# Performance work log

Measured on AMD Instinct MI355X. Metric: run time of the kernel, lower is better.

## Reference

```python
import jax, jax.numpy as jnp
import numpy as np

B, D_IN, D_OUT, H, E, K = 16384, 1024, 1024, 2048, 8, 2

def setup_inputs() -> dict:
    key = jax.random.key(0)
    ks = jax.random.split(key, 7)
    s_in = 1.0 / np.sqrt(D_IN)
    s_h = 1.0 / np.sqrt(H)
    return {
        "x": jax.random.normal(ks[0], (B, D_IN), dtype=jnp.float32),
        "router_W": jax.random.uniform(ks[1], (E, D_IN), jnp.float32, -s_in, s_in),
        "router_b": jax.random.uniform(ks[2], (E,), jnp.float32, -s_in, s_in),
        "W1": jax.random.uniform(ks[3], (E, H, D_IN), jnp.float32, -s_in, s_in),
        "b1": jax.random.uniform(ks[4], (E, H), jnp.float32, -s_in, s_in),
        "W2": jax.random.uniform(ks[5], (E, D_OUT, H), jnp.float32, -s_h, s_h),
        "b2": jax.random.uniform(ks[6], (E, D_OUT), jnp.float32, -s_h, s_h),
    }

def reference(x, router_W, router_b, W1, b1, W2, b2):
    # Router: softmax over experts, top-k selection, renormalize
    logits = x @ router_W.T + router_b                      # [B, E]
    router_probs = jax.nn.softmax(logits, axis=-1)          # [B, E]
    top_v, top_i = jax.lax.top_k(router_probs, K)           # [B, K]
    top_v = top_v / jnp.sum(top_v, axis=-1, keepdims=True)  # renormalized
    # Scatter top-k weights into dense [B, E] combine weights (zero elsewhere)
    b_idx = jnp.arange(x.shape[0])[:, None]
    combine = jnp.zeros_like(router_probs).at[b_idx, top_i].add(top_v)  # [B, E]
    # Dense per-expert MLP, combined with zero weights for unselected experts
    # (identical math to the original mask/gather/scatter loop)
    h = jax.nn.relu(jnp.einsum('bi,ehi->beh', x, W1) + b1)  # [B, E, H]
    y = jnp.einsum('beh,eoh->beo', h, W2) + b2              # [B, E, O]
    out = jnp.einsum('beo,be->bo', y, combine)              # [B, O]
    return out, router_probs
```

## Files before the change

kernel.cpp:

```cpp
#include <hip/hip_runtime.h>
#include <hip/hip_bf16.h>

#define Bsz  16384
#define Din  1024
#define Dout 1024
#define Hdim 2048
#define Ecnt 8
#define CNT_PAD 32

typedef _Float16 f16;
typedef _Float16 f16x8 __attribute__((ext_vector_type(8)));
typedef _Float16 f16x4 __attribute__((ext_vector_type(4)));
typedef float    f32x4 __attribute__((ext_vector_type(4)));

#define AS_GLOBAL __attribute__((address_space(1)))
#define AS_LDS    __attribute__((address_space(3)))

__device__ __forceinline__ void async_copy16(const void* gptr, void* lptr) {
    __builtin_amdgcn_global_load_lds(
        (const AS_GLOBAL unsigned int*)gptr,
        (AS_LDS unsigned int*)lptr, 16, 0, 0);
}

__global__ __launch_bounds__(256) void cast_kernel(
    const float* __restrict__ in, f16* __restrict__ out)
{
    int i = (blockIdx.x * 256 + threadIdx.x) * 4;
    float4 v = *(const float4*)(in + i);
    f16x4 o;
    o.x = (f16)v.x; o.y = (f16)v.y; o.z = (f16)v.z; o.w = (f16)v.w;
    *(f16x4*)(out + i) = o;
}

__global__ __launch_bounds__(256) void router_kernel(
    const float* __restrict__ x, const float* __restrict__ rW,
    const float* __restrict__ rb, float* __restrict__ probs_out,
    int* __restrict__ cnt, int* __restrict__ bucket, float* __restrict__ gates)
{
    __shared__ float s_rw[Ecnt * Din];
    __shared__ int   s_e[64];
    __shared__ float s_g[64];
    __shared__ int   s_lpos[64];
    __shared__ int   s_lcnt[Ecnt];
    __shared__ int   s_base[Ecnt];

    int t = threadIdx.x;
    if (t < Ecnt) s_lcnt[t] = 0;
    for (int i = t; i < Ecnt * Din; i += 256) s_rw[i] = rW[i];
    __syncthreads();

    int wid = t >> 6, lane = t & 63;

    float rbv[8];
    #pragma unroll
    for (int e = 0; e < 8; e++) rbv[e] = rb[e];

    #pragma unroll 2
    for (int tt = 0; tt < 8; tt++) {
        int li = wid * 8 + tt;
        int token = blockIdx.x * 32 + li;
        const float* xrow = x + (size_t)token * Din;

        float acc[8] = {0,0,0,0,0,0,0,0};
        #pragma unroll
        for (int i = 0; i < 4; i++) {
            float4 xv = *(const float4*)(xrow + i * 256 + lane * 4);
            #pragma unroll
            for (int e = 0; e < 8; e++) {
                float4 wv = *(const float4*)(s_rw + e * Din + i * 256 + lane * 4);
                acc[e] += xv.x * wv.x + xv.y * wv.y + xv.z * wv.z + xv.w * wv.w;
            }
        }
        #pragma unroll
        for (int e = 0; e < 8; e++) {
            #pragma unroll
            for (int m = 1; m < 64; m <<= 1) acc[e] += __shfl_xor(acc[e], m, 64);
        }

        float p[8], mx = -1e30f;
        #pragma unroll
        for (int e = 0; e < 8; e++) { p[e] = acc[e] + rbv[e]; mx = fmaxf(mx, p[e]); }
        float s = 0.f;
        #pragma unroll
        for (int e = 0; e < 8; e++) { p[e] = expf(p[e] - mx); s += p[e]; }
        float inv = 1.f / s;
        #pragma unroll
        for (int e = 0; e < 8; e++) p[e] *= inv;

        if (lane == 0) {
            float* po = probs_out + (size_t)token * Ecnt;
            #pragma unroll
            for (int e = 0; e < 8; e++) po[e] = p[e];
            int i0 = 0; float v0 = p[0];
            #pragma unroll
            for (int e = 1; e < 8; e++) if (p[e] > v0) { v0 = p[e]; i0 = e; }
            int i1 = -1; float v1 = -1e30f;
            #pragma unroll
            for (int e = 0; e < 8; e++) if (e != i0 && p[e] > v1) { v1 = p[e]; i1 = e; }
            float invs = 1.f / (v0 + v1);
            s_e[2 * li]     = i0;  s_g[2 * li]     = v0 * invs;
            s_e[2 * li + 1] = i1;  s_g[2 * li + 1] = v1 * invs;
        }
    }
    __syncthreads();

    if (t < 64) s_lpos[t] = atomicAdd(&s_lcnt[s_e[t]], 1);
    __syncthreads();
    if (t < Ecnt) s_base[t] = atomicAdd(&cnt[t * CNT_PAD], s_lcnt[t]);
    __syncthreads();
    if (t < 64) {
        int e = s_e[t];
        int pos = s_base[e] + s_lpos[t];
        int li = t >> 1;
        int token = blockIdx.x * 32 + li;
        bucket[e * Bsz + pos] = token * 2 + (t & 1);
        gates [e * Bsz + pos] = s_g[t];
    }
}

template<int Kd, bool G1>
__global__ __launch_bounds__(256) void moe_gemm(
    const f16* __restrict__ A, const f16* __restrict__ Wt,
    const float* __restrict__ bias, const int* __restrict__ cnt,
    const int* __restrict__ bucket, const float* __restrict__ gates,
    f16* __restrict__ hbuf, float* __restrict__ out, int Ndim)
{
    int e = blockIdx.z;
    int count = min(cnt[e * CNT_PAD], Bsz);
    int m0 = blockIdx.y * 128;
    if (m0 >= count) return;
    int n0 = blockIdx.x * 128;

    __shared__ alignas(16) f16 As[128 * 32];
    __shared__ alignas(16) f16 Bs[128 * 32];
    __shared__ int   s_rows[128];
    __shared__ float s_gates[128];

    int t = threadIdx.x;
    if (t < 128) {
        int pos = min(m0 + t, count - 1);
        s_rows[t] = bucket[e * Bsz + pos];
        if constexpr (!G1) s_gates[t] = gates[e * Bsz + pos];
    }
    __syncthreads();

    int wave = t >> 6, lane = t & 63;
    int scol = (lane & 3) * 8;

    const f16* agp[2];
    const f16* bgp[2];
    #pragma unroll
    for (int j = 0; j < 2; j++) {
        int srow = wave * 32 + j * 16 + (lane >> 2);
        int r = s_rows[srow];
        size_t arow = G1 ? (size_t)(r >> 1) : (size_t)r;
        agp[j] = A + arow * Kd + scol;
        bgp[j] = Wt + ((size_t)e * Ndim + (n0 + srow)) * (size_t)Kd + scol;
    }

    int m_w = (wave >> 1) * 64;
    int n_w = (wave & 1) * 64;
    int frow = lane & 15;
    int fk   = (lane >> 4) * 8;

    f32x4 acc[4][4] = {};

    for (int k0 = 0; k0 < Kd; k0 += 32) {
        #pragma unroll
        for (int j = 0; j < 2; j++) {
            async_copy16(agp[j], As + (wave * 32 + j * 16) * 32);
            async_copy16(bgp[j], Bs + (wave * 32 + j * 16) * 32);
            agp[j] += 32; bgp[j] += 32;
        }
        __syncthreads();

        f16x8 af[4], bfr[4];
        #pragma unroll
        for (int i = 0; i < 4; i++) {
            af[i]  = *(const f16x8*)(As + (m_w + i * 16 + frow) * 32 + fk);
            bfr[i] = *(const f16x8*)(Bs + (n_w + i * 16 + frow) * 32 + fk);
        }
        #pragma unroll
        for (int i = 0; i < 4; i++)
            #pragma unroll
            for (int jj = 0; jj < 4; jj++)
                acc[i][jj] = __builtin_amdgcn_mfma_f32_16x16x32_f16(
                    af[i], bfr[jj], acc[i][jj], 0, 0, 0);
        __syncthreads();
    }

    float bv[4];
    #pragma unroll
    for (int jj = 0; jj < 4; jj++)
        bv[jj] = bias[e * Ndim + n0 + n_w + jj * 16 + frow];

    #pragma unroll
    for (int i = 0; i < 4; i++) {
        int mbase = m_w + i * 16 + (lane >> 4) * 4;
        #pragma unroll
        for (int reg = 0; reg < 4; reg++) {
            int m = mbase + reg;
            if (m0 + m >= count) continue;
            int r = s_rows[m];
            if constexpr (G1) {
                f16* hrow = hbuf + (size_t)r * Hdim;
                #pragma unroll
                for (int jj = 0; jj < 4; jj++) {
                    int n = n0 + n_w + jj * 16 + frow;
                    float v = acc[i][jj][reg] + bv[jj];
                    hrow[n] = (f16)fmaxf(v, 0.f);
                }
            } else {
                int token = r >> 1;
                float g = s_gates[m];
                #pragma unroll
                for (int jj = 0; jj < 4; jj++) {
                    int n = n0 + n_w + jj * 16 + frow;
                    float v = g * (acc[i][jj][reg] + bv[jj]);
                    atomicAdd(&out[(size_t)token * Dout + n], v);
                }
            }
        }
    }
}

extern "C" void kernel_launch(void* const* d_in, const int* in_sizes, int n_in,
                              void* d_out, int out_size, void* d_ws, size_t ws_size,
                              hipStream_t stream) {
    const float* x   = (const float*)d_in[0];
    const float* rW  = (const float*)d_in[1];
    const float* rb  = (const float*)d_in[2];
    const float* W1  = (const float*)d_in[3];
    const float* b1  = (const float*)d_in[4];
    const float* W2  = (const float*)d_in[5];
    const float* b2  = (const float*)d_in[6];
    float* out   = (float*)d_out;
    float* probs = out + (size_t)Bsz * Dout;

    char* ws = (char*)d_ws;
    int*   cnt    = (int*)ws;
    int*   bucket = (int*)(ws + 0x1000);
    float* gates  = (float*)(ws + 0x90000);
    f16*   x16    = (f16*)(ws + 0x200000);
    f16*   w16    = (f16*)(ws + 0x2200000);
    f16*   hbuf   = (f16*)(ws + 0x4200000);

    hipMemsetAsync(cnt, 0, Ecnt * CNT_PAD * sizeof(int), stream);
    hipMemsetAsync(out, 0, (size_t)Bsz * Dout * sizeof(float), stream);

    cast_kernel<<<(Bsz * Din) / 1024, 256, 0, stream>>>(x, x16);
    cast_kernel<<<(Ecnt * Hdim * Din) / 1024, 256, 0, stream>>>(W1, w16);

    router_kernel<<<Bsz / 32, 256, 0, stream>>>(x, rW, rb, probs, cnt, bucket, gates);

    dim3 g1(Hdim / 128, Bsz / 128, Ecnt);
    moe_gemm<Din, true><<<g1, 256, 0, stream>>>(
        x16, w16, b1, cnt, bucket, gates, hbuf, out, Hdim);

    cast_kernel<<<(Ecnt * Dout * Hdim) / 1024, 256, 0, stream>>>(W2, w16);

    dim3 g2(Dout / 128, Bsz / 128, Ecnt);
    moe_gemm<Hdim, false><<<g2, 256, 0, stream>>>(
        hbuf, w16, b2, cnt, bucket, gates, hbuf, out, Dout);
}
```

Before: 718.6 us.

## Rewrite MoE GEMM with 256x256 tiles, double-buffered LDS and swizzled layout

Replaces the 128x128 tile, single-buffer MoE GEMM with a 256x256 tile over 512 threads and a K-step of 64. The LDS is double-buffered so the next tile's async loads are interleaved with MFMA phases, with explicit waitcnt and barriers. It also adds an XOR swizzle on the LDS columns to avoid bank conflicts, s_setprio around the MFMA bursts, and a 1D grid remapped so consecutive blocks spread across XCDs. The larger tile raises data reuse, but it uses 128 KB of LDS and many accumulator registers, and it wastes more work on partially filled expert tiles.

```diff
diff --git a/kernel.cpp b/kernel.cpp
--- a/kernel.cpp
+++ b/kernel.cpp
@@ -20,6 +20,11 @@
     __builtin_amdgcn_global_load_lds(
         (const AS_GLOBAL unsigned int*)gptr,
         (AS_LDS unsigned int*)lptr, 16, 0, 0);
+}
+
+__device__ __forceinline__ void bar() {
+    __builtin_amdgcn_s_barrier();
+    asm volatile("" ::: "memory");
 }
 
 __global__ __launch_bounds__(256) void cast_kernel(
@@ -119,25 +124,32 @@
 }
 
 template<int Kd, bool G1>
-__global__ __launch_bounds__(256) void moe_gemm(
+__global__ __launch_bounds__(512, 2) void moe_gemm(
     const f16* __restrict__ A, const f16* __restrict__ Wt,
     const float* __restrict__ bias, const int* __restrict__ cnt,
     const int* __restrict__ bucket, const float* __restrict__ gates,
     f16* __restrict__ hbuf, float* __restrict__ out, int Ndim)
 {
-    int e = blockIdx.z;
+    int nblk = (int)gridDim.x;
+    int lid = (int)blockIdx.x;
+    lid = (lid & 7) * (nblk >> 3) + (lid >> 3);
+    int gx = Ndim >> 8;
+    int bx = lid % gx;
+    int rem = lid / gx;
+    int by = rem & 63;
+    int e  = rem >> 6;
+
     int count = min(cnt[e * CNT_PAD], Bsz);
-    int m0 = blockIdx.y * 128;
+    int m0 = by * 256;
     if (m0 >= count) return;
-    int n0 = blockIdx.x * 128;
-
-    __shared__ alignas(16) f16 As[128 * 32];
-    __shared__ alignas(16) f16 Bs[128 * 32];
-    __shared__ int   s_rows[128];
-    __shared__ float s_gates[128];
+    int n0 = bx * 256;
+
+    __shared__ alignas(16) f16 lds[2 * 32768];
+    __shared__ int   s_rows[256];
+    __shared__ float s_gates[256];
 
     int t = threadIdx.x;
-    if (t < 128) {
+    if (t < 256) {
         int pos = min(m0 + t, count - 1);
         s_rows[t] = bucket[e * Bsz + pos];
         if constexpr (!G1) s_gates[t] = gates[e * Bsz + pos];
@@ -145,58 +157,149 @@
     __syncthreads();
 
     int wave = t >> 6, lane = t & 63;
-    int scol = (lane & 3) * 8;
-
-    const f16* agp[2];
-    const f16* bgp[2];
+    int wm = wave >> 2, wn = wave & 3;
+    int frow = lane & 15;
+    int fq   = lane >> 4;
+
+    int srow = t >> 3;
+    int sch  = t & 7;
+    const f16* aGp[4];
+    const f16* bGp[4];
     #pragma unroll
-    for (int j = 0; j < 2; j++) {
-        int srow = wave * 32 + j * 16 + (lane >> 2);
-        int r = s_rows[srow];
+    for (int u = 0; u < 4; u++) {
+        int trow = u * 64 + srow;
+        int r = s_rows[trow];
         size_t arow = G1 ? (size_t)(r >> 1) : (size_t)r;
-        agp[j] = A + arow * Kd + scol;
-        bgp[j] = Wt + ((size_t)e * Ndim + (n0 + srow)) * (size_t)Kd + scol;
-    }
-
-    int m_w = (wave >> 1) * 64;
-    int n_w = (wave & 1) * 64;
-    int frow = lane & 15;
-    int fk   = (lane >> 4) * 8;
-
-    f32x4 acc[4][4] = {};
-
-    for (int k0 = 0; k0 < Kd; k0 += 32) {
-        #pragma unroll
-        for (int j = 0; j < 2; j++) {
-            async_copy16(agp[j], As + (wave * 32 + j * 16) * 32);
-            async_copy16(bgp[j], Bs + (wave * 32 + j * 16) * 32);
-            agp[j] += 32; bgp[j] += 32;
-        }
-        __syncthreads();
-
-        f16x8 af[4], bfr[4];
-        #pragma unroll
-        for (int i = 0; i < 4; i++) {
-            af[i]  = *(const f16x8*)(As + (m_w + i * 16 + frow) * 32 + fk);
-            bfr[i] = *(const f16x8*)(Bs + (n_w + i * 16 + frow) * 32 + fk);
-        }
-        #pragma unroll
-        for (int i = 0; i < 4; i++)
-            #pragma unroll
-            for (int jj = 0; jj < 4; jj++)
-                acc[i][jj] = __builtin_amdgcn_mfma_f32_16x16x32_f16(
-                    af[i], bfr[jj], acc[i][jj], 0, 0, 0);
-        __syncthreads();
-    }
+        int c = sch ^ (trow & 7);
+        aGp[u] = A + arow * (size_t)Kd + c * 8;
+        bGp[u] = Wt + ((size_t)e * Ndim + (n0 + trow)) * (size_t)Kd + c * 8;
+    }
+
+#define LDSA(b) (lds + (b) * 32768)
+#define LDSB(b) (lds + (b) * 32768 + 16384)
+#define STAGE_A(u, kk, b) async_copy16(aGp[u] + (kk), LDSA(b) + (u) * 4096 + wave * 512)
+#define STAGE_B(u, kk, b) async_copy16(bGp[u] + (kk), LDSB(b) + (u) * 4096 + wave * 512)
+#define WAIT_LGKM0 do { asm volatile("s_waitcnt lgkmcnt(0)" ::: "memory"); \
+                        __builtin_amdgcn_sched_barrier(0); } while (0)
+#define WAIT_VM(n) do { asm volatile("s_waitcnt vmcnt(" #n ")" ::: "memory"); \
+                        __builtin_amdgcn_sched_barrier(0); } while (0)
+
+    int sw0 = ((fq    ) ^ (frow & 7)) * 8;
+    int sw1 = ((4 + fq) ^ (frow & 7)) * 8;
+    int aRowBase = (wm * 128 + frow) * 64;
+    int bRowBase = (wn * 64  + frow) * 64;
+
+    f32x4 acc[8][4] = {};
+    f16x8 bf[4][2];
+    f16x8 af[2][2];
+
+    STAGE_B(0, 0, 0); STAGE_B(1, 0, 0); STAGE_B(2, 0, 0); STAGE_B(3, 0, 0);
+    STAGE_A(0, 0, 0); STAGE_A(2, 0, 0); STAGE_A(1, 0, 0); STAGE_A(3, 0, 0);
+    WAIT_VM(2);
+    bar();
+
+    const int NT = Kd / 64;
+    for (int tt = 0; tt < NT; ++tt) {
+        const int c  = tt & 1;
+        const int nb = c ^ 1;
+        const int kN = (tt + 1) * 64;
+        const bool pf = (tt + 1 < NT);
+
+        #pragma unroll
+        for (int jj = 0; jj < 4; jj++) {
+            bf[jj][0] = *(const f16x8*)(LDSB(c) + bRowBase + jj * 1024 + sw0);
+            bf[jj][1] = *(const f16x8*)(LDSB(c) + bRowBase + jj * 1024 + sw1);
+        }
+        af[0][0] = *(const f16x8*)(LDSA(c) + aRowBase + 0 * 1024 + sw0);
+        af[0][1] = *(const f16x8*)(LDSA(c) + aRowBase + 0 * 1024 + sw1);
+        af[1][0] = *(const f16x8*)(LDSA(c) + aRowBase + 1 * 1024 + sw0);
+        af[1][1] = *(const f16x8*)(LDSA(c) + aRowBase + 1 * 1024 + sw1);
+        if (pf) { STAGE_B(0, kN, nb); STAGE_B(1, kN, nb); }
+        bar();
+        WAIT_LGKM0;
+        __builtin_amdgcn_s_setprio(1);
+        #pragma unroll
+        for (int jj = 0; jj < 4; jj++) {
+            acc[0][jj] = __builtin_amdgcn_mfma_f32_16x16x32_f16(af[0][0], bf[jj][0], acc[0][jj], 0, 0, 0);
+            acc[0][jj] = __builtin_amdgcn_mfma_f32_16x16x32_f16(af[0][1], bf[jj][1], acc[0][jj], 0, 0, 0);
+            acc[1][jj] = __builtin_amdgcn_mfma_f32_16x16x32_f16(af[1][0], bf[jj][0], acc[1][jj], 0, 0, 0);
+            acc[1][jj] = __builtin_amdgcn_mfma_f32_16x16x32_f16(af[1][1], bf[jj][1], acc[1][jj], 0, 0, 0);
+        }
+        __builtin_amdgcn_s_setprio(0);
+        bar();
+
+        af[0][0] = *(const f16x8*)(LDSA(c) + aRowBase + 2 * 1024 + sw0);
+        af[0][1] = *(const f16x8*)(LDSA(c) + aRowBase + 2 * 1024 + sw1);
+        af[1][0] = *(const f16x8*)(LDSA(c) + aRowBase + 3 * 1024 + sw0);
+        af[1][1] = *(const f16x8*)(LDSA(c) + aRowBase + 3 * 1024 + sw1);
+        if (pf) { STAGE_B(2, kN, nb); STAGE_B(3, kN, nb); }
+        bar();
+        WAIT_LGKM0;
+        __builtin_amdgcn_s_setprio(1);
+        #pragma unroll
+        for (int jj = 0; jj < 4; jj++) {
+            acc[2][jj] = __builtin_amdgcn_mfma_f32_16x16x32_f16(af[0][0], bf[jj][0], acc[2][jj], 0, 0, 0);
+            acc[2][jj] = __builtin_amdgcn_mfma_f32_16x16x32_f16(af[0][1], bf[jj][1], acc[2][jj], 0, 0, 0);
+            acc[3][jj] = __builtin_amdgcn_mfma_f32_16x16x32_f16(af[1][0], bf[jj][0], acc[3][jj], 0, 0, 0);
+            acc[3][jj] = __builtin_amdgcn_mfma_f32_16x16x32_f16(af[1][1], bf[jj][1], acc[3][jj], 0, 0, 0);
+        }
+        __builtin_amdgcn_s_setprio(0);
+        if (pf) { WAIT_VM(4); }
+        else    { WAIT_VM(0); }
+        bar();
+
+        af[0][0] = *(const f16x8*)(LDSA(c) + aRowBase + 4 * 1024 + sw0);
+        af[0][1] = *(const f16x8*)(LDSA(c) + aRowBase + 4 * 1024 + sw1);
+        af[1][0] = *(const f16x8*)(LDSA(c) + aRowBase + 5 * 1024 + sw0);
+        af[1][1] = *(const f16x8*)(LDSA(c) + aRowBase + 5 * 1024 + sw1);
+        if (pf) { STAGE_A(0, kN, nb); STAGE_A(2, kN, nb); }
+        bar();
+        WAIT_LGKM0;
+        __builtin_amdgcn_s_setprio(1);
+        #pragma unroll
+        for (int jj = 0; jj < 4; jj++) {
+            acc[4][jj] = __builtin_amdgcn_mfma_f32_16x16x32_f16(af[0][0], bf[jj][0], acc[4][jj], 0, 0, 0);
+            acc[4][jj] = __builtin_amdgcn_mfma_f32_16x16x32_f16(af[0][1], bf[jj][1], acc[4][jj], 0, 0, 0);
+            acc[5][jj] = __builtin_amdgcn_mfma_f32_16x16x32_f16(af[1][0], bf[jj][0], acc[5][jj], 0, 0, 0);
+            acc[5][jj] = __builtin_amdgcn_mfma_f32_16x16x32_f16(af[1][1], bf[jj][1], acc[5][jj], 0, 0, 0);
+        }
+        __builtin_amdgcn_s_setprio(0);
+        bar();
+
+        af[0][0] = *(const f16x8*)(LDSA(c) + aRowBase + 6 * 1024 + sw0);
+        af[0][1] = *(const f16x8*)(LDSA(c) + aRowBase + 6 * 1024 + sw1);
+        af[1][0] = *(const f16x8*)(LDSA(c) + aRowBase + 7 * 1024 + sw0);
+        af[1][1] = *(const f16x8*)(LDSA(c) + aRowBase + 7 * 1024 + sw1);
+        if (pf) { STAGE_A(1, kN, nb); STAGE_A(3, kN, nb); }
+        bar();
+        WAIT_LGKM0;
+        __builtin_amdgcn_s_setprio(1);
+        #pragma unroll
+        for (int jj = 0; jj < 4; jj++) {
+            acc[6][jj] = __builtin_amdgcn_mfma_f32_16x16x32_f16(af[0][0], bf[jj][0], acc[6][jj], 0, 0, 0);
+            acc[6][jj] = __builtin_amdgcn_mfma_f32_16x16x32_f16(af[0][1], bf[jj][1], acc[6][jj], 0, 0, 0);
+            acc[7][jj] = __builtin_amdgcn_mfma_f32_16x16x32_f16(af[1][0], bf[jj][0], acc[7][jj], 0, 0, 0);
+            acc[7][jj] = __builtin_amdgcn_mfma_f32_16x16x32_f16(af[1][1], bf[jj][1], acc[7][jj], 0, 0, 0);
+        }
+        __builtin_amdgcn_s_setprio(0);
+        if (pf) { WAIT_VM(2); }
+        bar();
+    }
+#undef LDSA
+#undef LDSB
+#undef STAGE_A
+#undef STAGE_B
+#undef WAIT_LGKM0
+#undef WAIT_VM
 
     float bv[4];
     #pragma unroll
     for (int jj = 0; jj < 4; jj++)
-        bv[jj] = bias[e * Ndim + n0 + n_w + jj * 16 + frow];
+        bv[jj] = bias[e * Ndim + n0 + wn * 64 + jj * 16 + frow];
 
     #pragma unroll
-    for (int i = 0; i < 4; i++) {
-        int mbase = m_w + i * 16 + (lane >> 4) * 4;
+    for (int i = 0; i < 8; i++) {
+        int mbase = wm * 128 + i * 16 + fq * 4;
         #pragma unroll
         for (int reg = 0; reg < 4; reg++) {
             int m = mbase + reg;
@@ -206,7 +309,7 @@
                 f16* hrow = hbuf + (size_t)r * Hdim;
                 #pragma unroll
                 for (int jj = 0; jj < 4; jj++) {
-                    int n = n0 + n_w + jj * 16 + frow;
+                    int n = n0 + wn * 64 + jj * 16 + frow;
                     float v = acc[i][jj][reg] + bv[jj];
                     hrow[n] = (f16)fmaxf(v, 0.f);
                 }
@@ -215,7 +318,7 @@
                 float g = s_gates[m];
                 #pragma unroll
                 for (int jj = 0; jj < 4; jj++) {
-                    int n = n0 + n_w + jj * 16 + frow;
+                    int n = n0 + wn * 64 + jj * 16 + frow;
                     float v = g * (acc[i][jj][reg] + bv[jj]);
                     atomicAdd(&out[(size_t)token * Dout + n], v);
                 }
@@ -253,13 +356,13 @@
 
     router_kernel<<<Bsz / 32, 256, 0, stream>>>(x, rW, rb, probs, cnt, bucket, gates);
 
-    dim3 g1(Hdim / 128, Bsz / 128, Ecnt);
-    moe_gemm<Din, true><<<g1, 256, 0, stream>>>(
+    int nb1 = (Hdim / 256) * (Bsz / 256) * Ecnt;
+    moe_gemm<Din, true><<<nb1, 512, 0, stream>>>(
         x16, w16, b1, cnt, bucket, gates, hbuf, out, Hdim);
 
     cast_kernel<<<(Ecnt * Dout * Hdim) / 1024, 256, 0, stream>>>(W2, w16);
 
-    dim3 g2(Dout / 128, Bsz / 128, Ecnt);
-    moe_gemm<Hdim, false><<<g2, 256, 0, stream>>>(
+    int nb2 = (Dout / 256) * (Bsz / 256) * Ecnt;
+    moe_gemm<Hdim, false><<<nb2, 512, 0, stream>>>(
         hbuf, w16, b2, cnt, bucket, gates, hbuf, out, Dout);
 }
```

Measured after the change: 738.1 us. 2.7% more time.
